# Kernel tuning notes

Measured on AMD Instinct MI355X. Metric: run time of the kernel, lower is better.

The kernel has to match this reference:

```python
import jax, jax.numpy as jnp
import numpy as np
from jax.scipy.linalg import solve_triangular

B, T, D = 4, 4096, 1024
H, R, P = 16, 32, 64          # n_heads, rank, d_head
RIDGE = 1e-3
POWER_K = 2
N_PI = 6                       # power-iteration steps


def setup_inputs() -> dict:
    key = jax.random.key(0)
    k0, k1, k2, k3 = jax.random.split(key, 4)
    h = jax.random.normal(k0, (B, T, D), dtype=jnp.float32)
    t_pref = (3 * T) // 4
    prefix_mask = jnp.concatenate(
        [jnp.ones((B, t_pref), jnp.float32), jnp.zeros((B, T - t_pref), jnp.float32)], axis=1)
    s = 1.0 / np.sqrt(D).astype(np.float32)
    Wk = jax.random.normal(k1, (H * R, D), dtype=jnp.float32) * s   # key_proj.weight
    Wq = jax.random.normal(k2, (H * R, D), dtype=jnp.float32) * s   # query_proj.weight
    Wv = jax.random.normal(k3, (H * P, D), dtype=jnp.float32) * s   # value_proj.weight
    eta = jnp.asarray(1.5, jnp.float32)
    ssn_gamma = jnp.asarray(1.0, jnp.float32)
    return {"h": h, "prefix_mask": prefix_mask, "Wk": Wk, "Wq": Wq, "Wv": Wv,
            "eta": eta, "ssn_gamma": ssn_gamma}


def _ska(h, prefix_mask, Wk, Wq, Wv, eta, ssn_gamma):
    b, t, _ = h.shape
    z = (h @ Wk.T).reshape(b, t, H, R)
    zq = (h @ Wq.T).reshape(b, t, H, R)
    v = (h @ Wv.T).reshape(b, t, H, P)

    m = prefix_mask[:, :, None, None]                               # [B,T,1,1]
    z_norms = jnp.linalg.norm(z, axis=-1, keepdims=True)            # [B,T,H,1]
    max_norm = jnp.clip(jnp.max(z_norms, axis=1, keepdims=True), 1e-6)
    z_f = z / max_norm
    zq_f = zq / max_norm

    z_m = z_f * m
    G = jnp.einsum('bthr,bths->bhrs', z_m, z_m)                     # [B,H,R,R]
    m_lag = (prefix_mask[:, :-1] * prefix_mask[:, 1:])[:, :, None, None]
    M_cov = jnp.einsum('bthr,bths->bhrs', z_f[:, 1:] * m_lag, z_f[:, :-1] * m_lag)
    C_v = jnp.einsum('bthp,bthr->bhpr', v * m, z_m)                 # [B,H,P,R]

    G_t = G + RIDGE * jnp.eye(R, dtype=jnp.float32)
    G_sym = 0.5 * (G_t + jnp.swapaxes(G_t, -1, -2))                 # robust-cholesky first attempt
    L = jnp.linalg.cholesky(G_sym)                                  # lower

    Y = solve_triangular(L, M_cov, lower=True)
    Aw_T = solve_triangular(L, jnp.swapaxes(Y, -1, -2), lower=True)
    A_w = jnp.swapaxes(Aw_T, -1, -2)                                # [B,H,R,R]

    # spectral normalization via power iteration (no-grad in original)
    A_sg = jax.lax.stop_gradient(A_w)
    vv = jnp.ones((b, H, R, 1), jnp.float32) / np.sqrt(R)
    for _ in range(N_PI):
        Av = A_sg @ vv
        u = Av / jnp.clip(jnp.linalg.norm(Av, axis=-2, keepdims=True), 1e-8)
        Atu = jnp.swapaxes(A_sg, -1, -2) @ u
        vv = Atu / jnp.clip(jnp.linalg.norm(Atu, axis=-2, keepdims=True), 1e-8)
    sigma_max = jnp.linalg.norm(A_sg @ vv, axis=-2)[..., 0]          # [B,H]
    scale = jnp.clip(sigma_max, 1.0)[..., None, None]
    A_w = A_w / scale
    gamma_safe = jnp.clip(ssn_gamma, 1.0, 1.5)
    A_w = A_w * gamma_safe

    # B_v = cholesky_solve(C_v^T, L)^T
    X = solve_triangular(L, jnp.swapaxes(C_v, -1, -2), lower=True)
    X = solve_triangular(jnp.swapaxes(L, -1, -2), X, lower=False)
    B_v = jnp.swapaxes(X, -1, -2)                                    # [B,H,P,R]

    zq_perm = jnp.transpose(zq_f, (0, 2, 3, 1))                      # [B,H,R,T]
    w_q = solve_triangular(L, zq_perm, lower=True)
    A_filt = A_w
    for _ in range(POWER_K - 1):
        A_filt = A_filt @ A_w
    w_f = A_filt @ w_q
    z_out = L @ w_f                                                   # [B,H,R,T]
    y_hat = jnp.transpose(B_v @ z_out, (0, 3, 1, 2))                  # [B,T,H,P]
    return eta * y_hat


def reference(h, prefix_mask, Wk, Wq, Wv, eta, ssn_gamma):
    return _ska(h, prefix_mask, Wk, Wq, Wv, eta, ssn_gamma)
```

## Files before the change

### kernel.cpp

```cpp
#include <hip/hip_runtime.h>

#define Tq 4096
#define Dq 1024
#define NCOL 2048
#define RIDGEC 1e-3f
#define PSTRIDE 4104

typedef float  f4_t  __attribute__((ext_vector_type(4)));
typedef __bf16 bf8_t __attribute__((ext_vector_type(8)));
typedef unsigned short us4_t __attribute__((ext_vector_type(4)));

typedef __attribute__((address_space(1))) const void* gas_t;
typedef __attribute__((address_space(3))) void* sas_t;

__device__ __forceinline__ unsigned short f2bf(float f){
    unsigned int u = __float_as_uint(f);
    u += 0x7fffu + ((u >> 16) & 1u);
    return (unsigned short)(u >> 16);
}
__device__ __forceinline__ float bf2f(unsigned short u){
    return __uint_as_float(((unsigned int)u) << 16);
}

__global__ __launch_bounds__(256) void k_prep(const float* __restrict__ h,
                                              const float* __restrict__ Wk,
                                              const float* __restrict__ Wq,
                                              const float* __restrict__ Wv,
                                              unsigned short* __restrict__ hbf,
                                              unsigned short* __restrict__ wbf){
    int bx = blockIdx.x;
    if (bx < 16384){
        size_t i = ((size_t)bx*256 + threadIdx.x)*4;
        float4 v = *(const float4*)(h + i);
        us4_t o; o.x=f2bf(v.x); o.y=f2bf(v.y); o.z=f2bf(v.z); o.w=f2bf(v.w);
        *(us4_t*)(hbf + i) = o;
    } else {
        size_t i = ((size_t)(bx - 16384)*256 + threadIdx.x)*4;
        int row = (int)(i >> 10), col = (int)(i & 1023);
        const float* s;
        if (row < 512)       s = Wk + (size_t)row*1024 + col;
        else if (row < 1024) s = Wq + (size_t)(row-512)*1024 + col;
        else                 s = Wv + (size_t)(row-1024)*1024 + col;
        float4 v = *(const float4*)s;
        us4_t o; o.x=f2bf(v.x); o.y=f2bf(v.y); o.z=f2bf(v.z); o.w=f2bf(v.w);
        *(us4_t*)(wbf + i) = o;
    }
}

__global__ __launch_bounds__(256) void k_gemm(const unsigned short* __restrict__ A,
                                              const unsigned short* __restrict__ Bw,
                                              unsigned short* __restrict__ zqv){
    __shared__ __align__(16) unsigned short As[128*32];
    __shared__ __align__(16) unsigned short Bs[128*32];
    const int tid = threadIdx.x, w = tid >> 6, lane = tid & 63;
    const int m0 = blockIdx.y*128, n0 = blockIdx.x*128;
    const int wm = (w >> 1)*64, wn = (w & 1)*64;
    const int row16 = lane & 15, klo = (lane >> 4)*8;

    f4_t acc[4][4];
#pragma unroll
    for (int i=0;i<4;++i)
#pragma unroll
        for (int j=0;j<4;++j) acc[i][j] = (f4_t){0.f,0.f,0.f,0.f};

    for (int k0 = 0; k0 < Dq; k0 += 32){
#pragma unroll
        for (int j=0;j<2;++j){
            int chunk = w*2 + j;
            int e = chunk*512 + lane*8;
            int r = e >> 5, c = e & 31;
            const unsigned short* ga = A  + (size_t)(m0 + r)*Dq + k0 + c;
            const unsigned short* gb = Bw + (size_t)(n0 + r)*Dq + k0 + c;
            __builtin_amdgcn_global_load_lds((gas_t)ga, (sas_t)&As[chunk*512], 16, 0, 0);
            __builtin_amdgcn_global_load_lds((gas_t)gb, (sas_t)&Bs[chunk*512], 16, 0, 0);
        }
        __syncthreads();
        bf8_t aF[4], bF[4];
#pragma unroll
        for (int i=0;i<4;++i) aF[i] = *(const bf8_t*)&As[(wm + i*16 + row16)*32 + klo];
#pragma unroll
        for (int j=0;j<4;++j) bF[j] = *(const bf8_t*)&Bs[(wn + j*16 + row16)*32 + klo];
#pragma unroll
        for (int i=0;i<4;++i)
#pragma unroll
            for (int j=0;j<4;++j)
                acc[i][j] = __builtin_amdgcn_mfma_f32_16x16x32_bf16(aF[i], bF[j], acc[i][j], 0, 0, 0);
        __syncthreads();
    }
#pragma unroll
    for (int i=0;i<4;++i){
#pragma unroll
        for (int j=0;j<4;++j){
            int col = n0 + wn + j*16 + row16;
            int rb  = m0 + wm + i*16 + (lane >> 4)*4;
#pragma unroll
            for (int q=0;q<4;++q)
                zqv[(size_t)(rb+q)*NCOL + col] = f2bf(acc[i][j][q]);
        }
    }
}

__global__ __launch_bounds__(256) void k_cov(const unsigned short* __restrict__ zqv,
                                             const float* __restrict__ mask,
                                             float* __restrict__ part){
    __shared__ float Zs[65*32];
    __shared__ float Vs[64*64];
    __shared__ float Msk[66];
    __shared__ float sMx[64];
    const int tid = threadIdx.x, w = tid >> 6, lane = tid & 63;
    const int c = blockIdx.x, bh = blockIdx.y, b = bh >> 4, h = bh & 15;
    const unsigned short* zb = zqv + (size_t)b*Tq*NCOL + h*32;
    const unsigned short* vb = zqv + (size_t)b*Tq*NCOL + 1024 + h*64;
    const float* mb = mask + (size_t)b*Tq;

    const bool isC = lane >= 32;
    const bool isM = (lane >= 16) && (lane < 32);
    const int li = isC ? (lane - 32) : (lane & 15);
    const int i0 = (li >> 2)*8, j0 = (li & 3)*8;
    const float* Xb = isC ? (Vs + i0) : (Zs + 32 + i0);
    const int xst = isC ? 64 : 32;
    const float* Yb = isM ? (Zs + j0) : (Zs + 32 + j0);
    const int slotbase = isC ? (2048 + i0*32 + j0) : ((isM ? 1024 : 0) + i0*32 + j0);

    float acc[8][8];
#pragma unroll
    for (int i=0;i<8;++i)
#pragma unroll
        for (int j=0;j<8;++j) acc[i][j] = 0.f;
    float mxl = 0.f;

    for (int t0 = c*512; t0 < c*512 + 512; t0 += 64){
        __syncthreads();
        for (int i = tid; i < 520; i += 256){
            int r = i >> 3, cc = (i & 7)*4;
            int t = t0 - 1 + r;
            float4 o;
            if (t >= 0){
                us4_t u = *(const us4_t*)(zb + (size_t)t*NCOL + cc);
                o.x = bf2f(u.x); o.y = bf2f(u.y); o.z = bf2f(u.z); o.w = bf2f(u.w);
            } else { o.x=0.f; o.y=0.f; o.z=0.f; o.w=0.f; }
            *(float4*)&Zs[r*32 + cc] = o;
        }
        for (int i = tid; i < 1024; i += 256){
            int rr = i >> 4, cc = (i & 15)*4;
            us4_t u = *(const us4_t*)(vb + (size_t)(t0 + rr)*NCOL + cc);
            float4 o; o.x=bf2f(u.x); o.y=bf2f(u.y); o.z=bf2f(u.z); o.w=bf2f(u.w);
            *(float4*)&Vs[rr*64 + cc] = o;
        }
        if (tid < 65){ int t = t0 - 1 + tid; Msk[tid] = (t >= 0) ? mb[t] : 0.f; }
        __syncthreads();
        if (tid < 64){
            const float4* pr = (const float4*)&Zs[(tid+1)*32];
            float s = 0.f;
#pragma unroll
            for (int q=0;q<8;++q){ float4 v = pr[q]; s += v.x*v.x + v.y*v.y + v.z*v.z + v.w*v.w; }
            mxl = fmaxf(mxl, s);
        }
#pragma unroll 2
        for (int tt = w; tt < 64; tt += 4){
            const float mt = Msk[tt+1], mp = Msk[tt];
            const float m2 = mt*mt, al = mt*mp;
            const float wgt = isM ? (al*al) : m2;
            const float* xp = Xb + tt*xst;
            const float* yp = Yb + tt*32;
            float4 x0 = *(const float4*)xp, x1 = *(const float4*)(xp + 4);
            float4 y0 = *(const float4*)yp, y1 = *(const float4*)(yp + 4);
            float xs[8] = {x0.x*wgt, x0.y*wgt, x0.z*wgt, x0.w*wgt,
                           x1.x*wgt, x1.y*wgt, x1.z*wgt, x1.w*wgt};
            float ys[8] = {y0.x, y0.y, y0.z, y0.w, y1.x, y1.y, y1.z, y1.w};
#pragma unroll
            for (int i=0;i<8;++i)
#pragma unroll
                for (int j=0;j<8;++j) acc[i][j] += xs[i]*ys[j];
        }
    }
    float* Acc = Vs;
    __syncthreads();
    if (tid < 64) sMx[tid] = mxl;
#pragma unroll
    for (int r = 0; r < 4; ++r){
        if (w == r){
            if (r == 0){
#pragma unroll
                for (int i=0;i<8;++i)
#pragma unroll
                    for (int j=0;j<8;++j) Acc[slotbase + i*32 + j] = acc[i][j];
            } else {
#pragma unroll
                for (int i=0;i<8;++i)
#pragma unroll
                    for (int j=0;j<8;++j) Acc[slotbase + i*32 + j] += acc[i][j];
            }
        }
        __syncthreads();
    }
    float* dst = part + ((size_t)c*64 + bh)*PSTRIDE;
    for (int i = tid; i < 4096; i += 256) dst[i] = Acc[i];
    if (tid == 0){
        float m = 0.f;
#pragma unroll
        for (int q=0;q<64;++q) m = fmaxf(m, sMx[q]);
        dst[4096] = m;
    }
}

__global__ __launch_bounds__(256) void k_solve(const float* __restrict__ part,
                                               const float* __restrict__ eta_p,
                                               const float* __restrict__ gam_p,
                                               unsigned short* __restrict__ Ebf){
    __shared__ float sM[1024], sC[2048], sGi[1024], sP[1024], sQ[1024], sT[1024];
    __shared__ float sAug[32*66];
    __shared__ float sv[32], su[32], sw[32], ssc[4];
    const int tid = threadIdx.x, bh = blockIdx.x;
    const size_t pb = (size_t)bh*PSTRIDE;

    float mxx = 0.f;
#pragma unroll
    for (int c = 0; c < 8; ++c) mxx = fmaxf(mxx, part[((size_t)c*64)*PSTRIDE + pb + 4096]);
    const float mn = fmaxf(sqrtf(mxx), 1e-6f);
    const float i1 = 1.f/mn, i2 = i1*i1;

    for (int i = tid; i < 1024; i += 256){
        float a0 = 0.f, a1 = 0.f;
        for (int c = 0; c < 8; ++c){
            const float* p = part + ((size_t)c*64)*PSTRIDE + pb;
            a0 += p[i]; a1 += p[1024 + i];
        }
        sT[i] = a0; sM[i] = a1*i2;
    }
    for (int i = tid; i < 2048; i += 256){
        float a = 0.f;
        for (int c = 0; c < 8; ++c) a += part[((size_t)c*64)*PSTRIDE + pb + 2048 + i];
        sC[i] = a*i1;
    }
    __syncthreads();
    for (int i = tid; i < 1024; i += 256){
        int r = i >> 5, s = i & 31;
        float g = 0.5f*(sT[i] + sT[s*32 + r])*i2 + (r == s ? RIDGEC : 0.f);
        sAug[r*66 + s] = g;
        sAug[r*66 + 32 + s] = (r == s) ? 1.f : 0.f;
    }
    __syncthreads();
    const int gi = tid >> 3, gj0 = (tid & 7)*8;
    for (int p = 0; p < 32; ++p){
        float pivd = sAug[p*66 + p];
        float f    = sAug[gi*66 + p];
        float rp[8];
#pragma unroll
        for (int jj = 0; jj < 8; ++jj) rp[jj] = sAug[p*66 + gj0 + jj];
        __syncthreads();
        float pinv = 1.f/pivd;
        if (gi == p){
#pragma unroll
            for (int jj = 0; jj < 8; ++jj) sAug[p*66 + gj0 + jj] = rp[jj]*pinv;
        } else {
            float fp = f*pinv;
#pragma unroll
            for (int jj = 0; jj < 8; ++jj) sAug[gi*66 + gj0 + jj] -= fp*rp[jj];
        }
        __syncthreads();
    }
    for (int i = tid; i < 1024; i += 256){
        int r = i >> 5, s = i & 31;
        sGi[i] = sAug[r*66 + 32 + s];
    }
    __syncthreads();
    {
        const int r = tid >> 3, s0 = (tid & 7)*4;
        float lrow[32];
#pragma unroll
        for (int q = 0; q < 8; ++q) *(float4*)&lrow[q*4] = *(const float4*)&sM[r*32 + q*4];
        float4 a = (float4){0.f,0.f,0.f,0.f};
        for (int k = 0; k < 32; ++k){
            float4 bb = *(const float4*)&sGi[k*32 + s0];
            a.x += lrow[k]*bb.x; a.y += lrow[k]*bb.y; a.z += lrow[k]*bb.z; a.w += lrow[k]*bb.w;
        }
        *(float4*)&sP[r*32 + s0] = a;
    }
    __syncthreads();
    {
        const int r = tid >> 3, s0 = (tid & 7)*4;
        float lrow[32];
#pragma unroll
        for (int q = 0; q < 8; ++q) *(float4*)&lrow[q*4] = *(const float4*)&sGi[r*32 + q*4];
        float4 a = (float4){0.f,0.f,0.f,0.f};
        for (int k = 0; k < 32; ++k){
            float4 bb = *(const float4*)&sP[k*32 + s0];
            a.x += lrow[k]*bb.x; a.y += lrow[k]*bb.y; a.z += lrow[k]*bb.z; a.w += lrow[k]*bb.w;
        }
        *(float4*)&sQ[r*32 + s0] = a;
    }
    __syncthreads();
    if (tid < 32) sv[tid] = 0.17677669529663687f;
    __syncthreads();
    for (int it = 0; it < 6; ++it){
        if (tid < 32){ float a = 0.f; for (int k = 0; k < 32; ++k) a += sQ[tid*32+k]*sv[k]; su[tid] = a; }
        __syncthreads();
        if (tid < 32){ float a = 0.f; for (int k = 0; k < 32; ++k) a += sM[k*32+tid]*su[k]; sw[tid] = a; }
        __syncthreads();
        if (tid < 32){
            float n2 = 0.f;
#pragma unroll
            for (int k = 0; k < 32; ++k) n2 += sw[k]*sw[k];
            sv[tid] = sw[tid] * (1.f/fmaxf(sqrtf(n2), 1e-8f));
        }
        __syncthreads();
    }
    if (tid < 32){ float a = 0.f; for (int k = 0; k < 32; ++k) a += sQ[tid*32+k]*sv[k]; su[tid] = a; }
    __syncthreads();
    if (tid < 32){ float a = 0.f; for (int k = 0; k < 32; ++k) a += sM[k*32+tid]*su[k]; sw[tid] = a; }
    __syncthreads();
    if (tid == 0){
        float n2 = 0.f;
        for (int k = 0; k < 32; ++k) n2 += sw[k]*sw[k];
        float sigma = sqrtf(sqrtf(n2));
        float gam = fminf(fmaxf(gam_p[0], 1.f), 1.5f);
        float s = gam/fmaxf(sigma, 1.f);
        ssc[0] = eta_p[0]*i1*s*s;
    }
    __syncthreads();
    {
        const int r = tid >> 3, s0 = (tid & 7)*4;
        float lrow[32];
#pragma unroll
        for (int q = 0; q < 8; ++q) *(float4*)&lrow[q*4] = *(const float4*)&sQ[r*32 + q*4];
        float4 a = (float4){0.f,0.f,0.f,0.f};
        for (int k = 0; k < 32; ++k){
            float4 bb = *(const float4*)&sP[k*32 + s0];
            a.x += lrow[k]*bb.x; a.y += lrow[k]*bb.y; a.z += lrow[k]*bb.z; a.w += lrow[k]*bb.w;
        }
        *(float4*)&sT[r*32 + s0] = a;
    }
    __syncthreads();
    {
        const float esc = ssc[0];
        const int r = tid >> 2, s0 = (tid & 3)*8;
        float lrow[32];
#pragma unroll
        for (int q = 0; q < 8; ++q) *(float4*)&lrow[q*4] = *(const float4*)&sC[r*32 + q*4];
        float4 a0 = (float4){0.f,0.f,0.f,0.f}, a1 = (float4){0.f,0.f,0.f,0.f};
        for (int k = 0; k < 32; ++k){
            float4 b0 = *(const float4*)&sT[k*32 + s0];
            float4 b1 = *(const float4*)&sT[k*32 + s0 + 4];
            a0.x += lrow[k]*b0.x; a0.y += lrow[k]*b0.y; a0.z += lrow[k]*b0.z; a0.w += lrow[k]*b0.w;
            a1.x += lrow[k]*b1.x; a1.y += lrow[k]*b1.y; a1.z += lrow[k]*b1.z; a1.w += lrow[k]*b1.w;
        }
        us4_t o0, o1;
        o0.x=f2bf(a0.x*esc); o0.y=f2bf(a0.y*esc); o0.z=f2bf(a0.z*esc); o0.w=f2bf(a0.w*esc);
        o1.x=f2bf(a1.x*esc); o1.y=f2bf(a1.y*esc); o1.z=f2bf(a1.z*esc); o1.w=f2bf(a1.w*esc);
        *(us4_t*)&Ebf[(size_t)bh*2048 + r*32 + s0]     = o0;
        *(us4_t*)&Ebf[(size_t)bh*2048 + r*32 + s0 + 4] = o1;
    }
}

__global__ __launch_bounds__(256) void k_outm(const unsigned short* __restrict__ zqv,
                                              const unsigned short* __restrict__ Ebf,
                                              float* __restrict__ out){
    __shared__ __align__(16) unsigned short Es[2048];
    const int tid = threadIdx.x, w = tid >> 6, lane = tid & 63;
    const int bh = blockIdx.y, b = bh >> 4, h = bh & 15;
    ((float4*)Es)[tid & 255] = ((const float4*)(Ebf + (size_t)bh*2048))[tid & 255];
    __syncthreads();

    const int row16 = lane & 15, klo = (lane >> 4)*8;
    const int t0 = blockIdx.x*128 + w*32;
    const unsigned short* zq = zqv + ((size_t)b*Tq + t0 + row16)*NCOL + 512 + h*32 + klo;
    bf8_t aF0 = *(const bf8_t*)zq;
    bf8_t aF1 = *(const bf8_t*)(zq + (size_t)16*NCOL);

    bf8_t bF[4];
#pragma unroll
    for (int j=0;j<4;++j) bF[j] = *(const bf8_t*)&Es[(j*16 + row16)*32 + klo];

    f4_t acc[2][4];
#pragma unroll
    for (int i=0;i<2;++i)
#pragma unroll
        for (int j=0;j<4;++j) acc[i][j] = (f4_t){0.f,0.f,0.f,0.f};
#pragma unroll
    for (int j=0;j<4;++j){
        acc[0][j] = __builtin_amdgcn_mfma_f32_16x16x32_bf16(aF0, bF[j], acc[0][j], 0, 0, 0);
        acc[1][j] = __builtin_amdgcn_mfma_f32_16x16x32_bf16(aF1, bF[j], acc[1][j], 0, 0, 0);
    }
    const int rbase = (lane >> 4)*4;
#pragma unroll
    for (int half=0; half<2; ++half){
#pragma unroll
        for (int j=0;j<4;++j){
            int col = h*64 + j*16 + row16;
#pragma unroll
            for (int q=0;q<4;++q){
                int t = t0 + half*16 + rbase + q;
                out[((size_t)b*Tq + t)*1024 + col] = acc[half][j][q];
            }
        }
    }
}

extern "C" void kernel_launch(void* const* d_in, const int* in_sizes, int n_in,
                              void* d_out, int out_size, void* d_ws, size_t ws_size,
                              hipStream_t stream) {
    const float* h    = (const float*)d_in[0];
    const float* mask = (const float*)d_in[1];
    const float* Wk   = (const float*)d_in[2];
    const float* Wq   = (const float*)d_in[3];
    const float* Wv   = (const float*)d_in[4];
    const float* eta  = (const float*)d_in[5];
    const float* gam  = (const float*)d_in[6];
    float* out = (float*)d_out;

    char* ws = (char*)d_ws;
    unsigned short* hbf = (unsigned short*)(ws);
    unsigned short* wbf = (unsigned short*)(ws + 33554432);
    unsigned short* zqv = (unsigned short*)(ws + 37748736);
    float*          part= (float*)         (ws + 104857600);
    unsigned short* Ebf = (unsigned short*)(ws + 113262592);

    k_prep <<<18432, 256, 0, stream>>>(h, Wk, Wq, Wv, hbf, wbf);
    k_gemm <<<dim3(16, 128), 256, 0, stream>>>(hbf, wbf, zqv);
    k_cov  <<<dim3(8, 64), 256, 0, stream>>>(zqv, mask, part);
    k_solve<<<64, 256, 0, stream>>>(part, eta, gam, Ebf);
    k_outm <<<dim3(32, 64), 256, 0, stream>>>(zqv, Ebf, out);
}
```

Measured before the change: 311.6 us.

## Rewrite projection GEMM with 256x256 tiles, LDS multi-buffering and swizzled reads

The bf16 projection GEMM moves from 128x128 tiles with single-buffered LDS and two barriers per k-step to 256x256 tiles with 512 threads. Each warp now computes a 128x64 sub-tile, and a four-slot LDS ring is prefetched with global_load_lds while MFMAs run, using s_setprio and vmcnt waits. The change also adds XOR-swizzled LDS addressing to avoid bank conflicts and a block-index swizzle for L2 locality. The aim is to hide global-load latency and raise arithmetic intensity, at the cost of 128KB of LDS, higher register pressure, and intricate hand-tuned synchronization.

```diff
diff --git a/kernel.cpp b/kernel.cpp
--- a/kernel.cpp
+++ b/kernel.cpp
@@ -47,55 +47,143 @@
     }
 }
 
-__global__ __launch_bounds__(256) void k_gemm(const unsigned short* __restrict__ A,
-                                              const unsigned short* __restrict__ Bw,
-                                              unsigned short* __restrict__ zqv){
-    __shared__ __align__(16) unsigned short As[128*32];
-    __shared__ __align__(16) unsigned short Bs[128*32];
+#define STAGE_A(UI, KC) do { \
+    const unsigned short* g_ = Abase + (KC); \
+    __builtin_amdgcn_global_load_lds((gas_t)(g_), (sas_t)&Abuf[(UI)*8192 + w*512], 16, 0, 0); \
+    __builtin_amdgcn_global_load_lds((gas_t)(g_ + 128*1024), (sas_t)&Abuf[(UI)*8192 + 4096 + w*512], 16, 0, 0); \
+} while(0)
+#define STAGE_B(UI, KC) do { \
+    const unsigned short* g_ = Bbase + (KC); \
+    __builtin_amdgcn_global_load_lds((gas_t)(g_), (sas_t)&Bbuf[(UI)*8192 + w*512], 16, 0, 0); \
+    __builtin_amdgcn_global_load_lds((gas_t)(g_ + 128*1024), (sas_t)&Bbuf[(UI)*8192 + 4096 + w*512], 16, 0, 0); \
+} while(0)
+#define FENCE() asm volatile("" ::: "memory")
+
+__global__ __launch_bounds__(512, 2) void k_gemm(const unsigned short* __restrict__ A,
+                                                 const unsigned short* __restrict__ Bw,
+                                                 unsigned short* __restrict__ zqv){
+    __shared__ __align__(16) unsigned short Abuf[4*8192];
+    __shared__ __align__(16) unsigned short Bbuf[4*8192];
     const int tid = threadIdx.x, w = tid >> 6, lane = tid & 63;
-    const int m0 = blockIdx.y*128, n0 = blockIdx.x*128;
-    const int wm = (w >> 1)*64, wn = (w & 1)*64;
-    const int row16 = lane & 15, klo = (lane >> 4)*8;
-
-    f4_t acc[4][4];
-#pragma unroll
-    for (int i=0;i<4;++i)
+    const int wr = w >> 2, wc = w & 3;
+    const int bid = blockIdx.x;
+    const int swz = (bid & 7)*64 + (bid >> 3);
+    const int m0 = (swz >> 3)*256, n0 = (swz & 7)*256;
+
+    const int u    = w*64 + (lane ^ ((lane >> 2) & 3));
+    const int urow = u >> 2, ucol = (u & 3)*8;
+    const unsigned short* Abase = A  + (size_t)(m0 + urow)*Dq + ucol;
+    const unsigned short* Bbase = Bw + (size_t)(n0 + urow)*Dq + ucol;
+
+    const int r16 = lane & 15;
+    const int kch = ((((lane >> 4)*16) ^ ((lane & 3) << 4)) >> 1);
+    const int aRd = (wr*128 + r16)*32 + kch;
+    const int bRd = (wc*64  + r16)*32 + kch;
+
+    f4_t acc[8][4];
+#pragma unroll
+    for (int i=0;i<8;++i)
 #pragma unroll
         for (int j=0;j<4;++j) acc[i][j] = (f4_t){0.f,0.f,0.f,0.f};
 
-    for (int k0 = 0; k0 < Dq; k0 += 32){
-#pragma unroll
-        for (int j=0;j<2;++j){
-            int chunk = w*2 + j;
-            int e = chunk*512 + lane*8;
-            int r = e >> 5, c = e & 31;
-            const unsigned short* ga = A  + (size_t)(m0 + r)*Dq + k0 + c;
-            const unsigned short* gb = Bw + (size_t)(n0 + r)*Dq + k0 + c;
-            __builtin_amdgcn_global_load_lds((gas_t)ga, (sas_t)&As[chunk*512], 16, 0, 0);
-            __builtin_amdgcn_global_load_lds((gas_t)gb, (sas_t)&Bs[chunk*512], 16, 0, 0);
-        }
-        __syncthreads();
-        bf8_t aF[4], bF[4];
-#pragma unroll
-        for (int i=0;i<4;++i) aF[i] = *(const bf8_t*)&As[(wm + i*16 + row16)*32 + klo];
-#pragma unroll
-        for (int j=0;j<4;++j) bF[j] = *(const bf8_t*)&Bs[(wn + j*16 + row16)*32 + klo];
-#pragma unroll
-        for (int i=0;i<4;++i)
-#pragma unroll
-            for (int j=0;j<4;++j)
-                acc[i][j] = __builtin_amdgcn_mfma_f32_16x16x32_bf16(aF[i], bF[j], acc[i][j], 0, 0, 0);
-        __syncthreads();
-    }
-#pragma unroll
-    for (int i=0;i<4;++i){
-#pragma unroll
-        for (int j=0;j<4;++j){
-            int col = n0 + wn + j*16 + row16;
-            int rb  = m0 + wm + i*16 + (lane >> 4)*4;
+    STAGE_A(0, 0);  STAGE_B(0, 0);
+    STAGE_A(1, 32); STAGE_B(1, 32);
+    asm volatile("s_waitcnt vmcnt(4)" ::: "memory");
+    __builtin_amdgcn_s_barrier(); FENCE();
+
+    bf8_t aF[4], bF[4];
+    for (int t = 0; t < 15; ++t){
+        const int p  = t & 1,  np = (t+1) & 1;
+        const int a0 = p*2, a1 = p*2 + 1;
+        const int kcN = (t+1)*64;
+
+#pragma unroll
+        for (int mi=0;mi<4;++mi) aF[mi] = *(const bf8_t*)&Abuf[a0*8192 + aRd + mi*512];
+#pragma unroll
+        for (int nj=0;nj<4;++nj) bF[nj] = *(const bf8_t*)&Bbuf[a0*8192 + bRd + nj*512];
+        STAGE_A(np*2, kcN);
+        __builtin_amdgcn_s_barrier(); FENCE();
+        __builtin_amdgcn_s_setprio(1);
+#pragma unroll
+        for (int mi=0;mi<4;++mi)
+#pragma unroll
+            for (int nj=0;nj<4;++nj)
+                acc[mi][nj] = __builtin_amdgcn_mfma_f32_16x16x32_bf16(aF[mi], bF[nj], acc[mi][nj], 0, 0, 0);
+        __builtin_amdgcn_s_setprio(0);
+        __builtin_amdgcn_s_barrier(); FENCE();
+
+#pragma unroll
+        for (int mi=0;mi<4;++mi) aF[mi] = *(const bf8_t*)&Abuf[a0*8192 + aRd + (mi+4)*512];
+        STAGE_B(np*2, kcN);
+        __builtin_amdgcn_s_barrier(); FENCE();
+        __builtin_amdgcn_s_setprio(1);
+#pragma unroll
+        for (int mi=0;mi<4;++mi)
+#pragma unroll
+            for (int nj=0;nj<4;++nj)
+                acc[mi+4][nj] = __builtin_amdgcn_mfma_f32_16x16x32_bf16(aF[mi], bF[nj], acc[mi+4][nj], 0, 0, 0);
+        __builtin_amdgcn_s_setprio(0);
+        asm volatile("s_waitcnt vmcnt(4)" ::: "memory");
+        __builtin_amdgcn_s_barrier(); FENCE();
+
+#pragma unroll
+        for (int mi=0;mi<4;++mi) aF[mi] = *(const bf8_t*)&Abuf[a1*8192 + aRd + mi*512];
+#pragma unroll
+        for (int nj=0;nj<4;++nj) bF[nj] = *(const bf8_t*)&Bbuf[a1*8192 + bRd + nj*512];
+        STAGE_A(np*2+1, kcN+32);
+        __builtin_amdgcn_s_barrier(); FENCE();
+        __builtin_amdgcn_s_setprio(1);
+#pragma unroll
+        for (int mi=0;mi<4;++mi)
+#pragma unroll
+            for (int nj=0;nj<4;++nj)
+                acc[mi][nj] = __builtin_amdgcn_mfma_f32_16x16x32_bf16(aF[mi], bF[nj], acc[mi][nj], 0, 0, 0);
+        __builtin_amdgcn_s_setprio(0);
+        __builtin_amdgcn_s_barrier(); FENCE();
+
+#pragma unroll
+        for (int mi=0;mi<4;++mi) aF[mi] = *(const bf8_t*)&Abuf[a1*8192 + aRd + (mi+4)*512];
+        STAGE_B(np*2+1, kcN+32);
+        __builtin_amdgcn_s_barrier(); FENCE();
+        __builtin_amdgcn_s_setprio(1);
+#pragma unroll
+        for (int mi=0;mi<4;++mi)
+#pragma unroll
+            for (int nj=0;nj<4;++nj)
+                acc[mi+4][nj] = __builtin_amdgcn_mfma_f32_16x16x32_bf16(aF[mi], bF[nj], acc[mi+4][nj], 0, 0, 0);
+        __builtin_amdgcn_s_setprio(0);
+        asm volatile("s_waitcnt vmcnt(4)" ::: "memory");
+        __builtin_amdgcn_s_barrier(); FENCE();
+    }
+
+    asm volatile("s_waitcnt vmcnt(0)" ::: "memory");
+    __builtin_amdgcn_s_barrier(); FENCE();
+#pragma unroll
+    for (int kh=0; kh<2; ++kh){
+        const int ui = 2 + kh;
+#pragma unroll
+        for (int nj=0;nj<4;++nj) bF[nj] = *(const bf8_t*)&Bbuf[ui*8192 + bRd + nj*512];
+#pragma unroll
+        for (int half=0; half<2; ++half){
+#pragma unroll
+            for (int mi=0;mi<4;++mi) aF[mi] = *(const bf8_t*)&Abuf[ui*8192 + aRd + (half*4+mi)*512];
+#pragma unroll
+            for (int mi=0;mi<4;++mi)
+#pragma unroll
+                for (int nj=0;nj<4;++nj)
+                    acc[half*4+mi][nj] = __builtin_amdgcn_mfma_f32_16x16x32_bf16(aF[mi], bF[nj], acc[half*4+mi][nj], 0, 0, 0);
+        }
+    }
+
+#pragma unroll
+    for (int mi=0;mi<8;++mi){
+#pragma unroll
+        for (int nj=0;nj<4;++nj){
+            const int col = n0 + wc*64 + nj*16 + r16;
+            const int rb  = m0 + wr*128 + mi*16 + (lane >> 4)*4;
 #pragma unroll
             for (int q=0;q<4;++q)
-                zqv[(size_t)(rb+q)*NCOL + col] = f2bf(acc[i][j][q]);
+                zqv[(size_t)(rb+q)*NCOL + col] = f2bf(acc[mi][nj][q]);
         }
     }
 }
@@ -417,7 +505,7 @@
     unsigned short* Ebf = (unsigned short*)(ws + 113262592);
 
     k_prep <<<18432, 256, 0, stream>>>(h, Wk, Wq, Wv, hbf, wbf);
-    k_gemm <<<dim3(16, 128), 256, 0, stream>>>(hbf, wbf, zqv);
+    k_gemm <<<dim3(512), 512, 0, stream>>>(hbf, wbf, zqv);
     k_cov  <<<dim3(8, 64), 256, 0, stream>>>(zqv, mask, part);
     k_solve<<<64, 256, 0, stream>>>(part, eta, gam, Ebf);
     k_outm <<<dim3(32, 64), 256, 0, stream>>>(zqv, Ebf, out);
```

After: 304.7 us. 2.2% less time.
